# Kernel tuning notes

Measured on AMD Instinct MI355X. Metric: run time of the kernel, lower is better.

The kernel has to match this reference:

```python
import jax, jax.numpy as jnp
import numpy as np
import math

H, W = 32, 32
HID = 256
K = 4
B = 16
DIN = 272
DFF = 1024
L = 2
NB = 7
IMG_H, IMG_W = 256, 256
LN_EPS = 1e-5


def _layernorm(x, g, b):
    m = jnp.mean(x, axis=-1, keepdims=True)
    v = jnp.var(x, axis=-1, keepdims=True)
    return (x - m) / jnp.sqrt(v + LN_EPS) * g + b


def _neighbor_mask(h, w, nb):
    # (h*w, h*w): 0 inside the nb x nb window around each query pixel, -inf outside
    rr = jnp.repeat(jnp.arange(h), w)
    cc = jnp.tile(jnp.arange(w), h)
    near = (jnp.abs(rr[:, None] - rr[None, :]) <= nb // 2) & (
        jnp.abs(cc[:, None] - cc[None, :]) <= nb // 2
    )
    return jnp.where(near, 0.0, -jnp.inf).astype(jnp.float32)


def _pos_embed(row_embed, col_embed):
    # pos[i*w + j] = concat(col_embed[j], row_embed[i])  -> (h*w, hid)
    h, nf = row_embed.shape
    w = col_embed.shape[0]
    pe = jnp.concatenate(
        [
            jnp.broadcast_to(col_embed[None, :, :], (h, w, nf)),
            jnp.broadcast_to(row_embed[:, None, :], (h, w, nf)),
        ],
        axis=-1,
    )
    return pe.reshape(h * w, 2 * nf)


def _resize_bilinear_ac(x, oh, ow):
    # nn.UpsamplingBilinear2d => align_corners=True
    b, c, h, w = x.shape
    ys = jnp.arange(oh) * ((h - 1) / (oh - 1))
    y0 = jnp.floor(ys).astype(jnp.int32)
    y1 = jnp.minimum(y0 + 1, h - 1)
    fy = (ys - y0).astype(x.dtype)
    x = x[:, :, y0, :] * (1 - fy)[None, None, :, None] + x[:, :, y1, :] * fy[None, None, :, None]
    xs = jnp.arange(ow) * ((w - 1) / (ow - 1))
    x0 = jnp.floor(xs).astype(jnp.int32)
    x1 = jnp.minimum(x0 + 1, w - 1)
    fx = (xs - x0).astype(x.dtype)
    x = x[:, :, :, x0] * (1 - fx) + x[:, :, :, x1] * fx
    return x


def _forward(query_features, matched_features, qW, qb, kvW, kvb, row_embed, col_embed,
             aggW, aggb, n1g, n1b, l1W, l1b, l2W, l2b, n2g, n2b, outW, outb):
    b, c_in, h, w = query_features.shape
    n = h * w
    # b c h w -> b (h w) c, then input projections
    qt = query_features.transpose(0, 2, 3, 1).reshape(b, n, c_in) @ qW + qb  # (b,n,hid)
    kt = matched_features.transpose(0, 1, 3, 4, 2).reshape(K, b, n, c_in) @ kvW + kvb  # (K,b,n,hid)

    pos = _pos_embed(row_embed, col_embed)  # (n, hid); broadcast over batch
    mask = _neighbor_mask(h, w, NB)  # (n, n)
    scale = 1.0 / math.sqrt(qt.shape[-1])

    x = qt
    for l in range(L):
        qp = (x + pos) * scale            # q gets pos embed then scaled
        kp = kt + pos                     # k gets pos embed; v is the raw matched tokens
        scores = jnp.einsum('bnc,kbmc->kbnm', qp, kp) + mask
        attn = jax.nn.softmax(scores, axis=-1)
        o = jnp.einsum('kbnm,kbmc->bnkc', attn, kt).reshape(b, n, K * HID)
        o = o @ aggW[l] + aggb[l]
        x = _layernorm(x + o, n1g[l], n1b[l])
        ff = jax.nn.relu(x @ l1W[l] + l1b[l]) @ l2W[l] + l2b[l]
        x = _layernorm(x + ff, n2g[l], n2b[l])

    recon_tokens = x @ outW + outb  # (b,n,c_in)
    recon = recon_tokens.reshape(b, h, w, c_in).transpose(0, 3, 1, 2)
    pred = jnp.sqrt(jnp.sum((recon - query_features) ** 2, axis=1, keepdims=True))
    pred = (pred - pred.min()) / (pred.max() - pred.min())
    pred = _resize_bilinear_ac(pred, IMG_H, IMG_W)
    return recon, pred


def setup_inputs() -> dict:
    key = jax.random.key(0)
    ks = jax.random.split(key, 12)

    def nrm(k, shape, scale=0.02):
        return jax.random.normal(k, shape, jnp.float32) * scale

    return {
        'query_features': jax.random.normal(ks[0], (B, DIN, H, W), jnp.float32),
        'matched_features': jax.random.normal(ks[1], (K, B, DIN, H, W), jnp.float32),
        'qW': nrm(ks[2], (DIN, HID)), 'qb': jnp.zeros((HID,), jnp.float32),
        'kvW': nrm(ks[3], (DIN, HID)), 'kvb': jnp.zeros((HID,), jnp.float32),
        'row_embed': jax.random.uniform(ks[4], (H, HID // 2), jnp.float32),
        'col_embed': jax.random.uniform(ks[5], (W, HID // 2), jnp.float32),
        'aggW': nrm(ks[6], (L, K * HID, HID)), 'aggb': jnp.zeros((L, HID), jnp.float32),
        'n1g': jnp.ones((L, HID), jnp.float32), 'n1b': jnp.zeros((L, HID), jnp.float32),
        'l1W': nrm(ks[7], (L, HID, DFF)), 'l1b': jnp.zeros((L, DFF), jnp.float32),
        'l2W': nrm(ks[8], (L, DFF, HID)), 'l2b': jnp.zeros((L, HID), jnp.float32),
        'n2g': jnp.ones((L, HID), jnp.float32), 'n2b': jnp.zeros((L, HID), jnp.float32),
        'outW': nrm(ks[9], (HID, DIN)), 'outb': jnp.zeros((DIN,), jnp.float32),
    }


def reference(query_features, matched_features, qW, qb, kvW, kvb, row_embed, col_embed,
              aggW, aggb, n1g, n1b, l1W, l1b, l2W, l2b, n2g, n2b, outW, outb):
    return _forward(query_features, matched_features, qW, qb, kvW, kvb, row_embed,
                    col_embed, aggW, aggb, n1g, n1b, l1W, l1b, l2W, l2b, n2g, n2b,
                    outW, outb)
```

## Files before the change

### kernel.cpp

```cpp
#include <hip/hip_runtime.h>
#include <hip/hip_bf16.h>
#include <math.h>

#define BATCH 16
#define NTOK 1024
#define HID 256
#define KMEM 4
#define DIN 272
#define DINP 288
#define DFF 1024
#define LN_EPS 1e-5f

using short8 = __attribute__((ext_vector_type(8))) short;
using short4v = __attribute__((ext_vector_type(4))) short;
using floatx4 = __attribute__((ext_vector_type(4))) float;

__device__ inline short f2bf(float f) {
  unsigned u = __builtin_bit_cast(unsigned, f);
  u += 0x7fff + ((u >> 16) & 1);
  return (short)(u >> 16);
}
__device__ inline float bf2f(short s) {
  unsigned u = ((unsigned)(unsigned short)s) << 16;
  return __builtin_bit_cast(float, u);
}

#define QSCALE 0.0625f

__global__ __launch_bounds__(256) void pos_kernel(
    const float* __restrict__ row_e, const float* __restrict__ col_e,
    float* __restrict__ pos) {
  int t = blockIdx.x;
  int j = threadIdx.x;
  float v = (j < 128) ? col_e[(t & 31) * 128 + j]
                      : row_e[(t >> 5) * 128 + (j - 128)];
  pos[t * 256 + j] = v;
}

__global__ __launch_bounds__(256) void tcvt_kernel(
    const float* __restrict__ qf, const float* __restrict__ mf,
    short* __restrict__ qf_t, short* __restrict__ mf_t) {
  __shared__ short tile[32][33];
  int slice = blockIdx.x >> 5;
  int t0 = (blockIdx.x & 31) * 32;
  int c0 = blockIdx.y * 32;
  int tx = threadIdx.x & 31, ty = threadIdx.x >> 5;
  const float* s;
  short* d;
  if (slice < 16) {
    s = qf + (long)slice * DIN * NTOK;
    d = qf_t + (long)slice * NTOK * DINP;
  } else {
    s = mf + (long)(slice - 16) * DIN * NTOK;
    d = mf_t + (long)(slice - 16) * NTOK * DINP;
  }
#pragma unroll
  for (int i = 0; i < 4; i++) {
    int c = c0 + ty + i * 8;
    float v = (c < DIN) ? s[(long)c * NTOK + t0 + tx] : 0.f;
    tile[ty + i * 8][tx] = f2bf(v);
  }
  __syncthreads();
  d += (long)t0 * DINP + c0;
#pragma unroll
  for (int i = 0; i < 4; i++) {
    int tl = ty + i * 8;
    d[(long)tl * DINP + tx] = tile[tx][tl];
  }
}

struct WtJob {
  const float* src;
  short* dst;
  int K, Kd, N, ntx, start;
};
struct WtJobs {
  WtJob j[9];
};

__global__ __launch_bounds__(256) void wt_cvt_all_kernel(WtJobs jobs) {
  __shared__ short tile[32][33];
  int bid = blockIdx.x;
  int ji = 0;
#pragma unroll
  for (int i = 1; i < 9; ++i)
    if (bid >= jobs.j[i].start) ji = i;
  const float* W = jobs.j[ji].src;
  short* Wt = jobs.j[ji].dst;
  int K = jobs.j[ji].K, Kd = jobs.j[ji].Kd, N = jobs.j[ji].N;
  int local = bid - jobs.j[ji].start;
  int n0 = (local % jobs.j[ji].ntx) * 32;
  int k0 = (local / jobs.j[ji].ntx) * 32;
  int tx = threadIdx.x & 31, ty8 = threadIdx.x >> 5;
#pragma unroll
  for (int i = 0; i < 4; i++) {
    int k = k0 + ty8 + i * 8;
    int n = n0 + tx;
    float v = (k < K && n < N) ? W[(long)k * N + n] : 0.f;
    tile[ty8 + i * 8][tx] = f2bf(v);
  }
  __syncthreads();
#pragma unroll
  for (int i = 0; i < 4; i++) {
    int n = n0 + ty8 + i * 8;
    int k = k0 + tx;
    if (n < N && k < Kd) Wt[(long)n * Kd + k] = tile[tx][ty8 + i * 8];
  }
}

template <int OUTMODE>
__global__ __launch_bounds__(256) void gemm2_kernel(
    const short* __restrict__ A, const short* __restrict__ Wt,
    const float* __restrict__ bias, float* __restrict__ Cf,
    short* __restrict__ Cs, int M, int N, int K, int gxn,
    short* __restrict__ ktp, short* __restrict__ ktv,
    const float* __restrict__ pos, const float* __restrict__ qfp,
    float* __restrict__ ppart) {
  __shared__ short As[2][64][40];
  __shared__ short Bs[2][128][40];
  __shared__ float part_s[64][2];
  int nwg = gridDim.x;
  int cpx = nwg >> 3;
  int bid = blockIdx.x;
  int h = (bid & 7) * cpx + (bid >> 3);
  int cx = h % gxn;
  int ry = h / gxn;
  int row0 = ry * 64, col0 = cx * 128;
  int tid = threadIdx.x;
  int w = tid >> 6, lane = tid & 63;
  int wrow = (w >> 1) * 32, wcol = (w & 1) * 64;
  int lcol = lane & 15, kg = lane >> 4;

  int arow = tid >> 2, ak = (tid & 3) * 8;
  int brow = tid >> 2, bk = (tid & 3) * 8;
  const short* Ab = A + (long)row0 * K;
  const short* Bb = Wt + (long)col0 * K;
  bool bv0 = (col0 + brow) < N;
  bool bv1 = (col0 + brow + 64) < N;

  const short8 z8 = (short8){0, 0, 0, 0, 0, 0, 0, 0};
  short8 ra, rb0, rb1;
  ra = *reinterpret_cast<const short8*>(&Ab[(long)arow * K + ak]);
  rb0 = bv0 ? *reinterpret_cast<const short8*>(&Bb[(long)brow * K + bk]) : z8;
  rb1 = bv1 ? *reinterpret_cast<const short8*>(&Bb[(long)(brow + 64) * K + bk])
            : z8;
  *reinterpret_cast<short8*>(&As[0][arow][ak]) = ra;
  *reinterpret_cast<short8*>(&Bs[0][brow][bk]) = rb0;
  *reinterpret_cast<short8*>(&Bs[0][brow + 64][bk]) = rb1;
  __syncthreads();

  floatx4 acc[2][4];
#pragma unroll
  for (int m = 0; m < 2; ++m)
#pragma unroll
    for (int n = 0; n < 4; ++n) acc[m][n] = (floatx4){0.f, 0.f, 0.f, 0.f};

  int NT = K >> 5;
  for (int t = 0; t < NT; ++t) {
    int cur = t & 1;
    if (t + 1 < NT) {
      int ko = (t + 1) << 5;
      ra = *reinterpret_cast<const short8*>(&Ab[(long)arow * K + ko + ak]);
      rb0 = bv0 ? *reinterpret_cast<const short8*>(&Bb[(long)brow * K + ko + bk])
                : z8;
      rb1 = bv1 ? *reinterpret_cast<const short8*>(
                      &Bb[(long)(brow + 64) * K + ko + bk])
                : z8;
    }
    short8 af[2], bf[4];
#pragma unroll
    for (int m = 0; m < 2; ++m)
      af[m] = *reinterpret_cast<const short8*>(
          &As[cur][wrow + m * 16 + lcol][kg * 8]);
#pragma unroll
    for (int n = 0; n < 4; ++n)
      bf[n] = *reinterpret_cast<const short8*>(
          &Bs[cur][wcol + n * 16 + lcol][kg * 8]);
#pragma unroll
    for (int m = 0; m < 2; ++m)
#pragma unroll
      for (int n = 0; n < 4; ++n)
        acc[m][n] = __builtin_amdgcn_mfma_f32_16x16x32_bf16(af[m], bf[n],
                                                            acc[m][n], 0, 0, 0);
    if (t + 1 < NT) {
      int nxt = cur ^ 1;
      *reinterpret_cast<short8*>(&As[nxt][arow][ak]) = ra;
      *reinterpret_cast<short8*>(&Bs[nxt][brow][bk]) = rb0;
      *reinterpret_cast<short8*>(&Bs[nxt][brow + 64][bk]) = rb1;
    }
    __syncthreads();
  }

  if (OUTMODE == 4) {
    int bb = row0 >> 10;
    int tb0 = (row0 & 1023) + wrow;
    float sqp[2][4] = {};
#pragma unroll
    for (int n = 0; n < 4; ++n) {
      int c = col0 + wcol + n * 16 + lcol;
      if (c < N) {
        float bv = bias[c];
#pragma unroll
        for (int m = 0; m < 2; ++m) {
          int tb = tb0 + m * 16 + kg * 4;
          long addr = ((long)bb * DIN + c) * 1024 + tb;
          float4 qv = *reinterpret_cast<const float4*>(&qfp[addr]);
          float4 ov;
          float v0 = acc[m][n][0] + bv;
          float v1 = acc[m][n][1] + bv;
          float v2 = acc[m][n][2] + bv;
          float v3 = acc[m][n][3] + bv;
          ov.x = v0;
          ov.y = v1;
          ov.z = v2;
          ov.w = v3;
          float d0 = v0 - qv.x, d1 = v1 - qv.y, d2 = v2 - qv.z, d3 = v3 - qv.w;
          sqp[m][0] = fmaf(d0, d0, sqp[m][0]);
          sqp[m][1] = fmaf(d1, d1, sqp[m][1]);
          sqp[m][2] = fmaf(d2, d2, sqp[m][2]);
          sqp[m][3] = fmaf(d3, d3, sqp[m][3]);
          *reinterpret_cast<float4*>(&Cf[addr]) = ov;
        }
      }
    }
#pragma unroll
    for (int m = 0; m < 2; ++m)
#pragma unroll
      for (int q = 0; q < 4; ++q) {
        float s = sqp[m][q];
        s += __shfl_xor(s, 1);
        s += __shfl_xor(s, 2);
        s += __shfl_xor(s, 4);
        s += __shfl_xor(s, 8);
        if (lcol == 0) part_s[wrow + m * 16 + kg * 4 + q][w & 1] = s;
      }
    __syncthreads();
    if (tid < 64)
      ppart[(long)cx * 16384 + row0 + tid] = part_s[tid][0] + part_s[tid][1];
    return;
  }

#pragma unroll
  for (int n = 0; n < 4; ++n) {
    int c = col0 + wcol + n * 16 + lcol;
    if (c >= N) continue;
    float bv = bias[c];
#pragma unroll
    for (int m = 0; m < 2; ++m) {
      int rbase = row0 + wrow + m * 16 + kg * 4;
      if (OUTMODE == 0) {
#pragma unroll
        for (int q = 0; q < 4; ++q)
          Cf[(long)(rbase + q) * N + c] = acc[m][n][q] + bv;
      } else if (OUTMODE == 1) {
#pragma unroll
        for (int q = 0; q < 4; ++q)
          Cs[(long)(rbase + q) * N + c] = f2bf(fmaxf(acc[m][n][q] + bv, 0.f));
      } else if (OUTMODE == 3) {
#pragma unroll
        for (int q = 0; q < 4; ++q) {
          float val = acc[m][n][q] + bv;
          Cf[(long)(rbase + q) * N + c] = val;
          Cs[(long)(rbase + q) * N + c] =
              f2bf((val + pos[((rbase + q) & 1023) * 256 + c]) * QSCALE);
        }
      } else {
        int slice = rbase >> 10, tbase = rbase & 1023;
        short4v vt;
#pragma unroll
        for (int q = 0; q < 4; ++q) {
          float val = acc[m][n][q] + bv;
          vt[q] = f2bf(val);
          ktp[(long)(rbase + q) * 256 + c] =
              f2bf(val + pos[(tbase + q) * 256 + c]);
        }
        *reinterpret_cast<short4v*>(
            &ktv[(long)slice * (256 * 1024) + (long)c * 1024 + tbase]) = vt;
      }
    }
  }
}

template <bool EX, bool EQ>
__global__ __launch_bounds__(256) void gemm_ln_kernel(
    const short* __restrict__ A, const short* __restrict__ Wt,
    const float* __restrict__ bias, const float* __restrict__ res,
    const float* __restrict__ g, const float* __restrict__ bta,
    float* __restrict__ xout, short* __restrict__ x16out,
    const float* __restrict__ pos, short* __restrict__ q16out, int K) {
  __shared__ short As[2][32][40];
  __shared__ short Bs[2][256][40];
  __shared__ float st_s[32][4];
  __shared__ float st_s2[32][4];
  int tid = threadIdx.x;
  int row0 = blockIdx.x * 32;
  int w = tid >> 6, lane = tid & 63, lcol = lane & 15, kg = lane >> 4;
  int arow = tid >> 2, ak = (tid & 3) * 8;
  int brow = tid >> 2, bk = (tid & 3) * 8;
  const short* Ab = A + (long)row0 * K;

  short8 ra, rb[4];
  if (tid < 128) ra = *reinterpret_cast<const short8*>(&Ab[(long)arow * K + ak]);
#pragma unroll
  for (int i = 0; i < 4; ++i)
    rb[i] = *reinterpret_cast<const short8*>(&Wt[(long)(brow + i * 64) * K + bk]);
  if (tid < 128) *reinterpret_cast<short8*>(&As[0][arow][ak]) = ra;
#pragma unroll
  for (int i = 0; i < 4; ++i)
    *reinterpret_cast<short8*>(&Bs[0][brow + i * 64][bk]) = rb[i];
  __syncthreads();

  floatx4 acc[2][4];
#pragma unroll
  for (int m = 0; m < 2; ++m)
#pragma unroll
    for (int n = 0; n < 4; ++n) acc[m][n] = (floatx4){0.f, 0.f, 0.f, 0.f};

  int NT = K >> 5;
  for (int t = 0; t < NT; ++t) {
    int cur = t & 1;
    if (t + 1 < NT) {
      int ko = (t + 1) << 5;
      if (tid < 128)
        ra = *reinterpret_cast<const short8*>(&Ab[(long)arow * K + ko + ak]);
#pragma unroll
      for (int i = 0; i < 4; ++i)
        rb[i] = *reinterpret_cast<const short8*>(
            &Wt[(long)(brow + i * 64) * K + ko + bk]);
    }
    short8 af[2], bf[4];
#pragma unroll
    for (int m = 0; m < 2; ++m)
      af[m] =
          *reinterpret_cast<const short8*>(&As[cur][m * 16 + lcol][kg * 8]);
#pragma unroll
    for (int n = 0; n < 4; ++n)
      bf[n] = *reinterpret_cast<const short8*>(
          &Bs[cur][w * 64 + n * 16 + lcol][kg * 8]);
#pragma unroll
    for (int m = 0; m < 2; ++m)
#pragma unroll
      for (int n = 0; n < 4; ++n)
        acc[m][n] = __builtin_amdgcn_mfma_f32_16x16x32_bf16(af[m], bf[n],
                                                            acc[m][n], 0, 0, 0);
    if (t + 1 < NT) {
      int nxt = cur ^ 1;
      if (tid < 128) *reinterpret_cast<short8*>(&As[nxt][arow][ak]) = ra;
#pragma unroll
      for (int i = 0; i < 4; ++i)
        *reinterpret_cast<short8*>(&Bs[nxt][brow + i * 64][bk]) = rb[i];
    }
    __syncthreads();
  }

  float val[2][4][4];
#pragma unroll
  for (int n = 0; n < 4; ++n) {
    int c = w * 64 + n * 16 + lcol;
    float bv = bias[c];
#pragma unroll
    for (int m = 0; m < 2; ++m) {
      int rbase = row0 + m * 16 + kg * 4;
#pragma unroll
      for (int q = 0; q < 4; ++q)
        val[m][n][q] = acc[m][n][q] + bv + res[(long)(rbase + q) * 256 + c];
    }
  }
  float s[2][4], s2[2][4];
#pragma unroll
  for (int m = 0; m < 2; ++m)
#pragma unroll
    for (int q = 0; q < 4; ++q) {
      float ss = 0.f, ss2 = 0.f;
#pragma unroll
      for (int n = 0; n < 4; ++n) {
        float v = val[m][n][q];
        ss += v;
        ss2 = fmaf(v, v, ss2);
      }
      ss += __shfl_xor(ss, 1);
      ss2 += __shfl_xor(ss2, 1);
      ss += __shfl_xor(ss, 2);
      ss2 += __shfl_xor(ss2, 2);
      ss += __shfl_xor(ss, 4);
      ss2 += __shfl_xor(ss2, 4);
      ss += __shfl_xor(ss, 8);
      ss2 += __shfl_xor(ss2, 8);
      s[m][q] = ss;
      s2[m][q] = ss2;
    }
  if (lcol == 0) {
#pragma unroll
    for (int m = 0; m < 2; ++m)
#pragma unroll
      for (int q = 0; q < 4; ++q) {
        st_s[m * 16 + kg * 4 + q][w] = s[m][q];
        st_s2[m * 16 + kg * 4 + q][w] = s2[m][q];
      }
  }
  __syncthreads();
#pragma unroll
  for (int m = 0; m < 2; ++m)
#pragma unroll
    for (int q = 0; q < 4; ++q) {
      int row = m * 16 + kg * 4 + q;
      float4 a4 = *reinterpret_cast<const float4*>(&st_s[row][0]);
      float4 b4 = *reinterpret_cast<const float4*>(&st_s2[row][0]);
      float S = (a4.x + a4.y) + (a4.z + a4.w);
      float S2 = (b4.x + b4.y) + (b4.z + b4.w);
      float mean = S * (1.f / 256.f);
      float var = S2 * (1.f / 256.f) - mean * mean;
      float inv = rsqrtf(var + LN_EPS);
#pragma unroll
      for (int n = 0; n < 4; ++n) {
        int c = w * 64 + n * 16 + lcol;
        float o = (val[m][n][q] - mean) * inv * g[c] + bta[c];
        long addr = (long)(row0 + row) * 256 + c;
        if (EX) xout[addr] = o;
        x16out[addr] = f2bf(o);
        if (EQ)
          q16out[addr] =
              f2bf((o + pos[((row0 + row) & 1023) * 256 + c]) * QSCALE);
      }
    }
}

__global__ __launch_bounds__(256) void attn_kernel(
    const short* __restrict__ q16, const short* __restrict__ ktp,
    const short* __restrict__ ktv, short* __restrict__ o) {
  __shared__ short QP_s[32][264];
  __shared__ float st_mx[32][4];
  __shared__ float st_sm[32][4];
  int h = blockIdx.x;
  int xcd = h & 7, jj = h >> 3;
  int sidx = xcd * 8 + (jj >> 5);
  int r = jj & 31;
  int b = sidx & 15, k = sidx >> 4;
  int tid = threadIdx.x;
  int w = tid >> 6, lane = tid & 63, lcol = lane & 15, kg = lane >> 4;

  int r0 = max(r - 3, 0), r1 = min(r + 3, 31);
  int nkr = r1 - r0 + 1, nm = nkr * 32;
  const short* qb = q16 + ((long)b * NTOK + r * 32) * HID;
  const short* ktpb = ktp + ((long)(k * BATCH + b)) * NTOK * HID;
  const short* ktvb = ktv + ((long)(k * BATCH + b)) * NTOK * HID;

#pragma unroll
  for (int p = 0; p < 4; ++p) {
    int chunk = p * 256 + tid;
    int row = chunk >> 5, c8 = (chunk & 31) * 8;
    short8 v = *reinterpret_cast<const short8*>(&qb[(long)row * HID + c8]);
    *reinterpret_cast<short8*>(&QP_s[row][c8]) = v;
  }
  __syncthreads();

  floatx4 acc[2][4];
#pragma unroll
  for (int m = 0; m < 2; ++m)
#pragma unroll
    for (int n = 0; n < 4; ++n) acc[m][n] = (floatx4){0.f, 0.f, 0.f, 0.f};

  int tokn[4];
#pragma unroll
  for (int n = 0; n < 4; ++n) {
    int nf = w * 4 + n;
    int krow = min(r0 + (nf >> 1), 31);
    tokn[n] = krow * 32 + ((nf & 1) << 4) + lcol;
  }
#pragma unroll
  for (int s = 0; s < 8; ++s) {
    short8 af0 = *reinterpret_cast<const short8*>(&QP_s[lcol][s * 32 + kg * 8]);
    short8 af1 =
        *reinterpret_cast<const short8*>(&QP_s[16 + lcol][s * 32 + kg * 8]);
#pragma unroll
    for (int n = 0; n < 4; ++n) {
      short8 bfr = *reinterpret_cast<const short8*>(
          &ktpb[(long)tokn[n] * HID + s * 32 + kg * 8]);
      acc[0][n] =
          __builtin_amdgcn_mfma_f32_16x16x32_bf16(af0, bfr, acc[0][n], 0, 0, 0);
      acc[1][n] =
          __builtin_amdgcn_mfma_f32_16x16x32_bf16(af1, bfr, acc[1][n], 0, 0, 0);
    }
  }

  const float NEG = -3.0e38f;
  float mx[2][4];
#pragma unroll
  for (int m = 0; m < 2; ++m)
#pragma unroll
    for (int q = 0; q < 4; ++q) {
      int rr = m * 16 + kg * 4 + q;
      float vmax = NEG;
#pragma unroll
      for (int n = 0; n < 4; ++n) {
        int col = (w * 4 + n) * 16 + lcol;
        int ck = col & 31;
        bool ok = (col < nm) && (ck - rr <= 3) && (rr - ck <= 3);
        float v = ok ? acc[m][n][q] : NEG;
        acc[m][n][q] = v;
        vmax = fmaxf(vmax, v);
      }
      vmax = fmaxf(vmax, __shfl_xor(vmax, 1));
      vmax = fmaxf(vmax, __shfl_xor(vmax, 2));
      vmax = fmaxf(vmax, __shfl_xor(vmax, 4));
      vmax = fmaxf(vmax, __shfl_xor(vmax, 8));
      mx[m][q] = vmax;
    }
  if (lcol == 0) {
#pragma unroll
    for (int m = 0; m < 2; ++m)
#pragma unroll
      for (int q = 0; q < 4; ++q) st_mx[m * 16 + kg * 4 + q][w] = mx[m][q];
  }
  __syncthreads();
  float sm[2][4];
#pragma unroll
  for (int m = 0; m < 2; ++m)
#pragma unroll
    for (int q = 0; q < 4; ++q) {
      int rr = m * 16 + kg * 4 + q;
      float4 v4 = *reinterpret_cast<const float4*>(&st_mx[rr][0]);
      float g = fmaxf(fmaxf(v4.x, v4.y), fmaxf(v4.z, v4.w));
      float ss = 0.f;
#pragma unroll
      for (int n = 0; n < 4; ++n) {
        float v = acc[m][n][q];
        float pv = (v > -1.0e30f) ? exp2f((v - g) * 1.4426950408889634f) : 0.f;
        acc[m][n][q] = pv;
        ss += pv;
      }
      ss += __shfl_xor(ss, 1);
      ss += __shfl_xor(ss, 2);
      ss += __shfl_xor(ss, 4);
      ss += __shfl_xor(ss, 8);
      sm[m][q] = ss;
    }
  if (lcol == 0) {
#pragma unroll
    for (int m = 0; m < 2; ++m)
#pragma unroll
      for (int q = 0; q < 4; ++q) st_sm[m * 16 + kg * 4 + q][w] = sm[m][q];
  }
  __syncthreads();
#pragma unroll
  for (int m = 0; m < 2; ++m)
#pragma unroll
    for (int q = 0; q < 4; ++q) {
      int rr = m * 16 + kg * 4 + q;
      float4 v4 = *reinterpret_cast<const float4*>(&st_sm[rr][0]);
      float rinv = 1.0f / (v4.x + v4.y + v4.z + v4.w);
#pragma unroll
      for (int n = 0; n < 4; ++n) {
        QP_s[rr][(w * 4 + n) * 16 + lcol] = f2bf(acc[m][n][q] * rinv);
      }
    }
  __syncthreads();

  floatx4 oacc[2][4];
#pragma unroll
  for (int m = 0; m < 2; ++m)
#pragma unroll
    for (int n = 0; n < 4; ++n) oacc[m][n] = (floatx4){0.f, 0.f, 0.f, 0.f};

  for (int kb = 0; kb < nkr; ++kb) {
    short8 ap0 = *reinterpret_cast<const short8*>(&QP_s[lcol][kb * 32 + kg * 8]);
    short8 ap1 =
        *reinterpret_cast<const short8*>(&QP_s[16 + lcol][kb * 32 + kg * 8]);
    int tokb = (r0 + kb) * 32;
#pragma unroll
    for (int n = 0; n < 4; ++n) {
      int ch = w * 64 + n * 16 + lcol;
      short8 bv = *reinterpret_cast<const short8*>(
          &ktvb[(long)ch * NTOK + tokb + kg * 8]);
      oacc[0][n] =
          __builtin_amdgcn_mfma_f32_16x16x32_bf16(ap0, bv, oacc[0][n], 0, 0, 0);
      oacc[1][n] =
          __builtin_amdgcn_mfma_f32_16x16x32_bf16(ap1, bv, oacc[1][n], 0, 0, 0);
    }
  }
#pragma unroll
  for (int m = 0; m < 2; ++m)
#pragma unroll
    for (int n = 0; n < 4; ++n) {
      int ch = w * 64 + n * 16 + lcol;
#pragma unroll
      for (int q = 0; q < 4; ++q) {
        int rr = m * 16 + kg * 4 + q;
        o[((long)b * NTOK + r * 32 + rr) * (KMEM * HID) + k * HID + ch] =
            f2bf(oacc[m][n][q]);
      }
    }
}

__global__ __launch_bounds__(256) void minmax_kernel(
    const float* __restrict__ ppart, float* __restrict__ pred_sq,
    float* __restrict__ mnmx) {
  int tid = threadIdx.x;
  float mn = INFINITY, mx = -INFINITY;
  for (int i = tid; i < BATCH * NTOK; i += 256) {
    float v = ppart[i] + ppart[16384 + i] + ppart[32768 + i];
    pred_sq[i] = v;
    float sv = sqrtf(v);
    mn = fminf(mn, sv);
    mx = fmaxf(mx, sv);
  }
#pragma unroll
  for (int off = 32; off > 0; off >>= 1) {
    mn = fminf(mn, __shfl_xor(mn, off));
    mx = fmaxf(mx, __shfl_xor(mx, off));
  }
  __shared__ float smn[4], smx[4];
  int wave = tid >> 6, lane = tid & 63;
  if (lane == 0) {
    smn[wave] = mn;
    smx[wave] = mx;
  }
  __syncthreads();
  if (tid == 0) {
    mn = fminf(fminf(smn[0], smn[1]), fminf(smn[2], smn[3]));
    mx = fmaxf(fmaxf(smx[0], smx[1]), fmaxf(smx[2], smx[3]));
    mnmx[0] = mn;
    mnmx[1] = mx;
  }
}

__global__ __launch_bounds__(256) void resize_kernel(
    const float* __restrict__ pred_sq, const float* __restrict__ mnmx,
    float* __restrict__ out) {
  long idx = (long)blockIdx.x * 256 + threadIdx.x;
  if (idx >= (long)BATCH * 256 * 256) return;
  int b = (int)(idx >> 16);
  int oy = (int)((idx >> 8) & 255), ox = (int)(idx & 255);
  float mn = mnmx[0], mx = mnmx[1];
  float inv = 1.0f / (mx - mn);
  float ys = oy * (31.0f / 255.0f);
  int y0 = (int)floorf(ys);
  int y1 = min(y0 + 1, 31);
  float fy = ys - (float)y0;
  float xs = ox * (31.0f / 255.0f);
  int x0 = (int)floorf(xs);
  int x1 = min(x0 + 1, 31);
  float fx = xs - (float)x0;
  const float* p = pred_sq + b * NTOK;
  float v00 = sqrtf(p[y0 * 32 + x0]), v01 = sqrtf(p[y0 * 32 + x1]);
  float v10 = sqrtf(p[y1 * 32 + x0]), v11 = sqrtf(p[y1 * 32 + x1]);
  float cA = v00 * (1.f - fy) + v10 * fy;
  float cB = v01 * (1.f - fy) + v11 * fy;
  float v = cA * (1.f - fx) + cB * fx;
  out[idx] = (v - mn) * inv;
}

extern "C" void kernel_launch(void* const* d_in, const int* in_sizes, int n_in,
                              void* d_out, int out_size, void* d_ws,
                              size_t ws_size, hipStream_t stream) {
  const float* qf = (const float*)d_in[0];
  const float* mf = (const float*)d_in[1];
  const float* qW = (const float*)d_in[2];
  const float* qb = (const float*)d_in[3];
  const float* kvW = (const float*)d_in[4];
  const float* kvb = (const float*)d_in[5];
  const float* row_e = (const float*)d_in[6];
  const float* col_e = (const float*)d_in[7];
  const float* aggW = (const float*)d_in[8];
  const float* aggb = (const float*)d_in[9];
  const float* n1g = (const float*)d_in[10];
  const float* n1b = (const float*)d_in[11];
  const float* l1W = (const float*)d_in[12];
  const float* l1b = (const float*)d_in[13];
  const float* l2W = (const float*)d_in[14];
  const float* l2b = (const float*)d_in[15];
  const float* n2g = (const float*)d_in[16];
  const float* n2b = (const float*)d_in[17];
  const float* outW = (const float*)d_in[18];
  const float* outb = (const float*)d_in[19];

  float* out = (float*)d_out;
  float* recon = out;
  float* pred = out + (long)BATCH * DIN * NTOK;

  float* ws = (float*)d_ws;
  float* pos = ws;
  float* x = pos + 262144;
  short* x16 = (short*)(x + 4194304);
  short* q16 = x16 + 4194304;
  short* ktp = q16 + 4194304;
  short* ktv = ktp + 16777216;
  short* buf16 = ktv + 16777216;
  float* tmp256 = (float*)(buf16 + 16777216);
  short* wt = (short*)(tmp256 + 4194304);
  short* wt_agg0 = wt;
  short* wt_agg1 = wt_agg0 + 262144;
  short* wt_l1_0 = wt_agg1 + 262144;
  short* wt_l1_1 = wt_l1_0 + 262144;
  short* wt_l2_0 = wt_l1_1 + 262144;
  short* wt_l2_1 = wt_l2_0 + 262144;
  short* wt_out = wt_l2_1 + 262144;
  short* wt_q = wt_out + 69632;
  short* wt_kv = wt_q + 73728;
  float* pred_part = (float*)(wt_kv + 73728);
  float* pred_sq = pred_part + 49152;
  float* mnmx = pred_sq + 16384;
  short* qf_t = ktp;
  short* mf_t = buf16;

  pos_kernel<<<NTOK, 256, 0, stream>>>(row_e, col_e, pos);

  {
    WtJobs jobs;
    jobs.j[0] = {aggW, wt_agg0, 1024, 1024, 256, 8, 0};
    jobs.j[1] = {aggW + 262144, wt_agg1, 1024, 1024, 256, 8, 256};
    jobs.j[2] = {l1W, wt_l1_0, 256, 256, 1024, 32, 512};
    jobs.j[3] = {l1W + 262144, wt_l1_1, 256, 256, 1024, 32, 768};
    jobs.j[4] = {l2W, wt_l2_0, 1024, 1024, 256, 8, 1024};
    jobs.j[5] = {l2W + 262144, wt_l2_1, 1024, 1024, 256, 8, 1280};
    jobs.j[6] = {outW, wt_out, 256, 256, 272, 9, 1536};
    jobs.j[7] = {qW, wt_q, 272, 288, 256, 8, 1608};
    jobs.j[8] = {kvW, wt_kv, 272, 288, 256, 8, 1680};
    wt_cvt_all_kernel<<<1752, 256, 0, stream>>>(jobs);
  }

  tcvt_kernel<<<dim3(2560, 9), 256, 0, stream>>>(qf, mf, qf_t, mf_t);

  gemm2_kernel<3><<<512, 256, 0, stream>>>(
      qf_t, wt_q, qb, x, q16, BATCH * NTOK, HID, DINP, 2, nullptr, nullptr,
      pos, nullptr, nullptr);
  gemm2_kernel<2><<<2048, 256, 0, stream>>>(
      mf_t, wt_kv, kvb, nullptr, nullptr, KMEM * BATCH * NTOK, HID, DINP, 2,
      ktp, ktv, pos, nullptr, nullptr);

  for (int l = 0; l < 2; l++) {
    attn_kernel<<<2048, 256, 0, stream>>>(q16, ktp, ktv, buf16);
    gemm_ln_kernel<true, false><<<512, 256, 0, stream>>>(
        buf16, l ? wt_agg1 : wt_agg0, aggb + l * 256, x, n1g + l * 256,
        n1b + l * 256, x, x16, nullptr, nullptr, KMEM * HID);
    gemm2_kernel<1><<<2048, 256, 0, stream>>>(
        x16, l ? wt_l1_1 : wt_l1_0, l1b + l * 1024, nullptr, buf16,
        BATCH * NTOK, DFF, HID, 8, nullptr, nullptr, nullptr, nullptr,
        nullptr);
    if (l == 0) {
      gemm_ln_kernel<true, true><<<512, 256, 0, stream>>>(
          buf16, wt_l2_0, l2b, x, n2g, n2b, x, x16, pos, q16, DFF);
    } else {
      gemm_ln_kernel<false, false><<<512, 256, 0, stream>>>(
          buf16, wt_l2_1, l2b + 256, x, n2g + 256, n2b + 256, x, x16, nullptr,
          nullptr, DFF);
    }
  }

  gemm2_kernel<4><<<768, 256, 0, stream>>>(
      x16, wt_out, outb, recon, nullptr, BATCH * NTOK, DIN, HID, 3, nullptr,
      nullptr, nullptr, qf, pred_part);
  minmax_kernel<<<1, 256, 0, stream>>>(pred_part, pred_sq, mnmx);
  resize_kernel<<<(BATCH * 256 * 256) / 256, 256, 0, stream>>>(pred_sq, mnmx,
                                                               pred);
}
```

Baseline: 425.9 us.

## Fuse FFN up-projection, ReLU and down-projection with LayerNorm into one kernel

Replaces the separate FFN1 GEMM and the FFN2+LayerNorm GEMM with a single kernel. Each 32-row block keeps its input tile in shared memory, computes the hidden activations in 256-wide chunks, applies bias and ReLU into LDS, and accumulates the down-projection directly. This removes the write and re-read of the 16Kx1024 bf16 hidden buffer and one launch per layer. In exchange, weights are read straight from global memory with no LDS staging or prefetch, and each block rereads the full W1 and W2, which may make the kernel latency-bound.

```diff
diff --git a/kernel.cpp b/kernel.cpp
--- a/kernel.cpp
+++ b/kernel.cpp
@@ -358,6 +358,165 @@
   for (int n = 0; n < 4; ++n) {
     int c = w * 64 + n * 16 + lcol;
     float bv = bias[c];
+#pragma unroll
+    for (int m = 0; m < 2; ++m) {
+      int rbase = row0 + m * 16 + kg * 4;
+#pragma unroll
+      for (int q = 0; q < 4; ++q)
+        val[m][n][q] = acc[m][n][q] + bv + res[(long)(rbase + q) * 256 + c];
+    }
+  }
+  float s[2][4], s2[2][4];
+#pragma unroll
+  for (int m = 0; m < 2; ++m)
+#pragma unroll
+    for (int q = 0; q < 4; ++q) {
+      float ss = 0.f, ss2 = 0.f;
+#pragma unroll
+      for (int n = 0; n < 4; ++n) {
+        float v = val[m][n][q];
+        ss += v;
+        ss2 = fmaf(v, v, ss2);
+      }
+      ss += __shfl_xor(ss, 1);
+      ss2 += __shfl_xor(ss2, 1);
+      ss += __shfl_xor(ss, 2);
+      ss2 += __shfl_xor(ss2, 2);
+      ss += __shfl_xor(ss, 4);
+      ss2 += __shfl_xor(ss2, 4);
+      ss += __shfl_xor(ss, 8);
+      ss2 += __shfl_xor(ss2, 8);
+      s[m][q] = ss;
+      s2[m][q] = ss2;
+    }
+  if (lcol == 0) {
+#pragma unroll
+    for (int m = 0; m < 2; ++m)
+#pragma unroll
+      for (int q = 0; q < 4; ++q) {
+        st_s[m * 16 + kg * 4 + q][w] = s[m][q];
+        st_s2[m * 16 + kg * 4 + q][w] = s2[m][q];
+      }
+  }
+  __syncthreads();
+#pragma unroll
+  for (int m = 0; m < 2; ++m)
+#pragma unroll
+    for (int q = 0; q < 4; ++q) {
+      int row = m * 16 + kg * 4 + q;
+      float4 a4 = *reinterpret_cast<const float4*>(&st_s[row][0]);
+      float4 b4 = *reinterpret_cast<const float4*>(&st_s2[row][0]);
+      float S = (a4.x + a4.y) + (a4.z + a4.w);
+      float S2 = (b4.x + b4.y) + (b4.z + b4.w);
+      float mean = S * (1.f / 256.f);
+      float var = S2 * (1.f / 256.f) - mean * mean;
+      float inv = rsqrtf(var + LN_EPS);
+#pragma unroll
+      for (int n = 0; n < 4; ++n) {
+        int c = w * 64 + n * 16 + lcol;
+        float o = (val[m][n][q] - mean) * inv * g[c] + bta[c];
+        long addr = (long)(row0 + row) * 256 + c;
+        if (EX) xout[addr] = o;
+        x16out[addr] = f2bf(o);
+        if (EQ)
+          q16out[addr] =
+              f2bf((o + pos[((row0 + row) & 1023) * 256 + c]) * QSCALE);
+      }
+    }
+}
+
+template <bool EX, bool EQ>
+__global__ __launch_bounds__(256) void ffn_kernel(
+    const short* __restrict__ A, const short* __restrict__ W1,
+    const float* __restrict__ b1, const short* __restrict__ W2,
+    const float* __restrict__ b2, const float* __restrict__ res,
+    const float* __restrict__ g, const float* __restrict__ bta,
+    float* __restrict__ xout, short* __restrict__ x16out,
+    const float* __restrict__ pos, short* __restrict__ q16out) {
+  __shared__ short As[32][264];
+  __shared__ short Hs[32][264];
+  __shared__ float st_s[32][4];
+  __shared__ float st_s2[32][4];
+  int tid = threadIdx.x;
+  int row0 = blockIdx.x * 32;
+  int w = tid >> 6, lane = tid & 63, lcol = lane & 15, kg = lane >> 4;
+
+  const short* Ab = A + (long)row0 * HID;
+#pragma unroll
+  for (int p = 0; p < 4; ++p) {
+    int chunk = p * 256 + tid;
+    int row = chunk >> 5, c8 = (chunk & 31) * 8;
+    *reinterpret_cast<short8*>(&As[row][c8]) =
+        *reinterpret_cast<const short8*>(&Ab[(long)row * HID + c8]);
+  }
+  __syncthreads();
+
+  floatx4 acc[2][4];
+#pragma unroll
+  for (int m = 0; m < 2; ++m)
+#pragma unroll
+    for (int n = 0; n < 4; ++n) acc[m][n] = (floatx4){0.f, 0.f, 0.f, 0.f};
+
+  for (int c = 0; c < 4; ++c) {
+    int hbase = c * 256 + w * 64;
+    floatx4 facc[2][4];
+#pragma unroll
+    for (int m = 0; m < 2; ++m)
+#pragma unroll
+      for (int n = 0; n < 4; ++n) facc[m][n] = (floatx4){0.f, 0.f, 0.f, 0.f};
+#pragma unroll
+    for (int ks = 0; ks < 8; ++ks) {
+      short8 af0 =
+          *reinterpret_cast<const short8*>(&As[lcol][ks * 32 + kg * 8]);
+      short8 af1 =
+          *reinterpret_cast<const short8*>(&As[16 + lcol][ks * 32 + kg * 8]);
+#pragma unroll
+      for (int nf = 0; nf < 4; ++nf) {
+        short8 bf = *reinterpret_cast<const short8*>(
+            &W1[(long)(hbase + nf * 16 + lcol) * HID + ks * 32 + kg * 8]);
+        facc[0][nf] =
+            __builtin_amdgcn_mfma_f32_16x16x32_bf16(af0, bf, facc[0][nf], 0, 0, 0);
+        facc[1][nf] =
+            __builtin_amdgcn_mfma_f32_16x16x32_bf16(af1, bf, facc[1][nf], 0, 0, 0);
+      }
+    }
+    __syncthreads();
+#pragma unroll
+    for (int nf = 0; nf < 4; ++nf) {
+      float bv = b1[hbase + nf * 16 + lcol];
+      int wcol = w * 64 + nf * 16 + lcol;
+#pragma unroll
+      for (int m = 0; m < 2; ++m)
+#pragma unroll
+        for (int q = 0; q < 4; ++q)
+          Hs[m * 16 + kg * 4 + q][wcol] =
+              f2bf(fmaxf(facc[m][nf][q] + bv, 0.f));
+    }
+    __syncthreads();
+#pragma unroll
+    for (int ks = 0; ks < 8; ++ks) {
+      short8 ah0 =
+          *reinterpret_cast<const short8*>(&Hs[lcol][ks * 32 + kg * 8]);
+      short8 ah1 =
+          *reinterpret_cast<const short8*>(&Hs[16 + lcol][ks * 32 + kg * 8]);
+#pragma unroll
+      for (int nf = 0; nf < 4; ++nf) {
+        short8 bf = *reinterpret_cast<const short8*>(
+            &W2[(long)(w * 64 + nf * 16 + lcol) * DFF + c * 256 + ks * 32 +
+                kg * 8]);
+        acc[0][nf] =
+            __builtin_amdgcn_mfma_f32_16x16x32_bf16(ah0, bf, acc[0][nf], 0, 0, 0);
+        acc[1][nf] =
+            __builtin_amdgcn_mfma_f32_16x16x32_bf16(ah1, bf, acc[1][nf], 0, 0, 0);
+      }
+    }
+  }
+
+  float val[2][4][4];
+#pragma unroll
+  for (int n = 0; n < 4; ++n) {
+    int c = w * 64 + n * 16 + lcol;
+    float bv = b2[c];
 #pragma unroll
     for (int m = 0; m < 2; ++m) {
       int rbase = row0 + m * 16 + kg * 4;
@@ -733,17 +892,13 @@
     gemm_ln_kernel<true, false><<<512, 256, 0, stream>>>(
         buf16, l ? wt_agg1 : wt_agg0, aggb + l * 256, x, n1g + l * 256,
         n1b + l * 256, x, x16, nullptr, nullptr, KMEM * HID);
-    gemm2_kernel<1><<<2048, 256, 0, stream>>>(
-        x16, l ? wt_l1_1 : wt_l1_0, l1b + l * 1024, nullptr, buf16,
-        BATCH * NTOK, DFF, HID, 8, nullptr, nullptr, nullptr, nullptr,
-        nullptr);
     if (l == 0) {
-      gemm_ln_kernel<true, true><<<512, 256, 0, stream>>>(
-          buf16, wt_l2_0, l2b, x, n2g, n2b, x, x16, pos, q16, DFF);
+      ffn_kernel<true, true><<<512, 256, 0, stream>>>(
+          x16, wt_l1_0, l1b, wt_l2_0, l2b, x, n2g, n2b, x, x16, pos, q16);
     } else {
-      gemm_ln_kernel<false, false><<<512, 256, 0, stream>>>(
-          buf16, wt_l2_1, l2b + 256, x, n2g + 256, n2b + 256, x, x16, nullptr,
-          nullptr, DFF);
+      ffn_kernel<false, false><<<512, 256, 0, stream>>>(
+          x16, wt_l1_1, l1b + 1024, wt_l2_1, l2b + 256, x, n2g + 256,
+          n2b + 256, x, x16, nullptr, nullptr);
     }
   }
 
```

Result: slower. 484.4 us (+13.7%).
